# Performance work log

Measured on AMD Instinct MI355X. Metric: run time of the kernel, lower is better.

## Reference

```python
import jax, jax.numpy as jnp
import numpy as np

B = 32; SEQ = 900; GRID = 30; PFX = 16; D = 512
H = 8; HD = 64; WS = 3; SS = 1
NW = (GRID // WS) ** 2; N = WS * WS
INTER = 1536  # find_multiple(round(4.0*512*2/3), 256)
EPS = 1e-5
SCALE = HD ** -0.5


def _rel_pos_index():
    coords = np.stack(np.meshgrid(np.arange(WS), np.arange(WS), indexing='ij')).reshape(2, -1)
    rel = (coords[:, :, None] - coords[:, None, :]).transpose(1, 2, 0).copy()
    rel[:, :, 0] += WS - 1
    rel[:, :, 1] += WS - 1
    rel[:, :, 0] *= 2 * WS - 1
    return rel.sum(-1)  # [N, N]


def _attn_mask():
    img = np.zeros((GRID, GRID))
    cnt = 0
    sl = (slice(0, -WS), slice(-WS, -SS), slice(-SS, None))
    for h in sl:
        for w in sl:
            img[h, w] = cnt
            cnt += 1
    mw = img.reshape(GRID // WS, WS, GRID // WS, WS).transpose(0, 2, 1, 3).reshape(-1, N)
    diff = mw[:, None, :] - mw[:, :, None]
    return np.where(diff != 0, -100.0, 0.0).astype(np.float32)  # [nW, N, N]


REL_IDX = _rel_pos_index()
MASK = _attn_mask()


def rms_norm(x):
    xf = x.astype(jnp.float32)
    v = jnp.mean(xf * xf, -1, keepdims=True)
    return (xf * jax.lax.rsqrt(v + EPS)).astype(x.dtype)


def swiglu(x, gu_w, down_w):
    gu = x @ gu_w.T
    gate, up = gu[..., :INTER], gu[..., INTER:]
    return (jax.nn.silu(gate) * up) @ down_w.T


def setup_inputs() -> dict:
    key = jax.random.key(0)
    ks = jax.random.split(key, 8)
    s = 0.02
    return {
        'hidden_states': jax.random.normal(ks[0], (B, PFX + SEQ, D), jnp.float32),
        'qkv_w': jax.random.normal(ks[1], (3 * D, D), jnp.float32) * s,
        'qkv_b': jnp.zeros((3 * D,), jnp.float32),
        'proj_w': jax.random.normal(ks[2], (D, D), jnp.float32) * s,
        'proj_b': jnp.zeros((D,), jnp.float32),
        'rel_bias': jax.random.normal(ks[3], ((2 * WS - 1) ** 2, H), jnp.float32) * s,
        'gu_w': jax.random.normal(ks[4], (2 * INTER, D), jnp.float32) * s,
        'down_w': jax.random.normal(ks[5], (D, INTER), jnp.float32) * s,
        'pgu_w': jax.random.normal(ks[6], (2 * INTER, D), jnp.float32) * s,
        'pdown_w': jax.random.normal(ks[7], (D, INTER), jnp.float32) * s,
    }


def reference(hidden_states, qkv_w, qkv_b, proj_w, proj_b, rel_bias, gu_w, down_w, pgu_w, pdown_w):
    hs = hidden_states
    prefix = hs[:, :PFX]                                     # [B, 16, D]
    grid = hs[:, PFX:] + jnp.mean(prefix, 1, keepdims=True)  # broadcast prefix mean
    x = grid.reshape(B, GRID, GRID, D)
    residual = x
    # cyclic shift
    x = jnp.roll(x, (-SS, -SS), (1, 2))
    # window partition -> [B*nW, N, D]
    xw = x.reshape(B, GRID // WS, WS, GRID // WS, WS, D).transpose(0, 1, 3, 2, 4, 5).reshape(B * NW, N, D)
    qkv = (xw @ qkv_w.T + qkv_b).reshape(B * NW, N, 3, H, HD).transpose(2, 0, 3, 1, 4)
    q, k, v = qkv[0] * SCALE, qkv[1], qkv[2]                 # [B*nW, H, N, HD]
    attn = jnp.einsum('whid,whjd->whij', q, k)
    bias = rel_bias[jnp.asarray(REL_IDX).reshape(-1)].reshape(N, N, H).transpose(2, 0, 1)
    attn = attn + bias[None]
    attn = attn.reshape(B, NW, H, N, N) + jnp.asarray(MASK)[None, :, None]
    attn = jax.nn.softmax(attn.reshape(B * NW, H, N, N), -1)
    out = jnp.einsum('whij,whjd->whid', attn, v).transpose(0, 2, 1, 3).reshape(B * NW, N, D)
    out = out @ proj_w.T + proj_b
    # window reverse + reverse shift
    x = out.reshape(B, GRID // WS, GRID // WS, WS, WS, D).transpose(0, 1, 3, 2, 4, 5).reshape(B, GRID, GRID, D)
    x = jnp.roll(x, (SS, SS), (1, 2))
    x = rms_norm(residual.reshape(B, SEQ, D) + x.reshape(B, SEQ, D))
    prefix = rms_norm(prefix + swiglu(prefix, pgu_w, pdown_w))
    hs = jnp.concatenate([prefix, x], 1)
    return rms_norm(hs + swiglu(hs, gu_w, down_w))
```

## Files before the change

### kernel.cpp

```cpp
#include <hip/hip_runtime.h>
#include <cstdint>
#include <cstddef>

typedef float f32x4 __attribute__((ext_vector_type(4)));
typedef short s16x8 __attribute__((ext_vector_type(8)));
typedef short s16x4 __attribute__((ext_vector_type(4)));

#define DEV static __device__ __forceinline__

DEV float bf2f(short s) {
  union { unsigned u; float f; } c;
  c.u = ((unsigned)(unsigned short)s) << 16;
  return c.f;
}
DEV short f2bf(float f) {
  union { float f; unsigned u; } c;
  c.f = f;
  unsigned r = c.u + 0x7fffu + ((c.u >> 16) & 1u);
  return (short)(r >> 16);
}
DEV float wave_allsum(float v) {
#pragma unroll
  for (int off = 32; off > 0; off >>= 1) v += __shfl_xor(v, off, 64);
  return v;
}
DEV void gload_lds16(const void* g, void* l) {
  __builtin_amdgcn_global_load_lds(
      (const __attribute__((address_space(1))) void*)g,
      (__attribute__((address_space(3))) void*)l, 16, 0, 0);
}
DEV float silu_f(float g) { return g / (1.f + __expf(-g)); }

DEV int xcd_swizzle(int orig, int nwg) {
  int q = nwg >> 3, r = nwg & 7;
  int xcd = orig & 7, pos = orig >> 3;
  return (xcd < r ? xcd * (q + 1) : r * (q + 1) + (xcd - r) * q) + pos;
}

DEV void sync_phase() {
  asm volatile("s_waitcnt vmcnt(0)" ::: "memory");
  __builtin_amdgcn_s_barrier();
  __builtin_amdgcn_sched_barrier(0);
}

enum { EPI_BF16 = 0, EPI_BIAS_BF16 = 1, EPI_SCATTER = 4, EPI_GU = 6 };

template <int EPI>
__global__ __launch_bounds__(512, 2) void gemm8(
    const short* __restrict__ A, const short* __restrict__ W,
    const float* __restrict__ bias, void* __restrict__ outp,
    int M, int N, int K)
{
  __shared__ short lds[65536];
  const int tid = threadIdx.x;
  const int wid = tid >> 6, lane = tid & 63;
  const int wr = wid >> 2, wc = wid & 3;
  const int nwg = gridDim.x * gridDim.y;
  const int orig = blockIdx.y * gridDim.x + blockIdx.x;
  const int wg = xcd_swizzle(orig, nwg);
  const int bx = wg % gridDim.x, by = wg / gridDim.x;
  const int row0 = by * 256;
  const int c0 = bx * 256;

  f32x4 acc[8][4];
#pragma unroll
  for (int m = 0; m < 8; ++m)
#pragma unroll
    for (int n = 0; n < 4; ++n) acc[m][n] = f32x4{0.f, 0.f, 0.f, 0.f};

  const int srow = tid >> 3;
  const int k8s = (tid & 7) ^ (srow & 7);
  const short* aub[4];
  const short* bub[4];
#pragma unroll
  for (int u = 0; u < 4; ++u) {
    aub[u] = A + (size_t)(row0 + u * 64 + srow) * K + k8s * 8;
    bub[u] = W + (size_t)(c0 + u * 64 + srow) * K + k8s * 8;
  }
  const int ldw = wid * 512;

#define SA(d, u, kt) gload_lds16(aub[u] + (kt), &lds[(d)*16384 + (u)*4096 + ldw])
#define SB(d, u, kt) gload_lds16(bub[u] + (kt), &lds[32768 + (d)*16384 + (u)*4096 + ldw])
#define GATE(VN)                                              \
  asm volatile("s_waitcnt vmcnt(" #VN ")" ::: "memory");      \
  __builtin_amdgcn_s_barrier();                               \
  __builtin_amdgcn_sched_barrier(0);

  const int kg0 = (lane >> 4) ^ (lane & 7);
  const int kg1 = (4 + (lane >> 4)) ^ (lane & 7);
  const int aoff = (wr * 128 + (lane & 15)) * 64;
  const int boff = 32768 + (wc * 64 + (lane & 15)) * 64;

#define READ_B(d)                                                              \
  _Pragma("unroll") for (int n = 0; n < 4; ++n) {                              \
    bfr[0][n] = *(const s16x8*)&lds[(d)*16384 + boff + n * 1024 + kg0 * 8];    \
    bfr[1][n] = *(const s16x8*)&lds[(d)*16384 + boff + n * 1024 + kg1 * 8];    \
  }
#define DO_PHASE(d, p)                                                         \
  do {                                                                         \
    s16x8 a00 = *(const s16x8*)&lds[(d)*16384 + aoff + (2*(p))*1024 + kg0*8];  \
    s16x8 a01 = *(const s16x8*)&lds[(d)*16384 + aoff + (2*(p))*1024 + kg1*8];  \
    s16x8 a10 = *(const s16x8*)&lds[(d)*16384 + aoff + (2*(p)+1)*1024 + kg0*8];\
    s16x8 a11 = *(const s16x8*)&lds[(d)*16384 + aoff + (2*(p)+1)*1024 + kg1*8];\
    __builtin_amdgcn_s_setprio(1);                                             \
    _Pragma("unroll") for (int n = 0; n < 4; ++n)                              \
      acc[2*(p)][n] = __builtin_amdgcn_mfma_f32_16x16x32_bf16(a00, bfr[0][n], acc[2*(p)][n], 0, 0, 0); \
    _Pragma("unroll") for (int n = 0; n < 4; ++n)                              \
      acc[2*(p)+1][n] = __builtin_amdgcn_mfma_f32_16x16x32_bf16(a10, bfr[0][n], acc[2*(p)+1][n], 0, 0, 0); \
    _Pragma("unroll") for (int n = 0; n < 4; ++n)                              \
      acc[2*(p)][n] = __builtin_amdgcn_mfma_f32_16x16x32_bf16(a01, bfr[1][n], acc[2*(p)][n], 0, 0, 0); \
    _Pragma("unroll") for (int n = 0; n < 4; ++n)                              \
      acc[2*(p)+1][n] = __builtin_amdgcn_mfma_f32_16x16x32_bf16(a11, bfr[1][n], acc[2*(p)+1][n], 0, 0, 0); \
    __builtin_amdgcn_s_setprio(0);                                             \
  } while (0)

  SB(0, 0, 0); SB(0, 1, 0); SB(0, 2, 0); SB(0, 3, 0);
  SA(0, 0, 0); SA(0, 2, 0); SA(0, 1, 0); SA(0, 3, 0);

  const int NT = K >> 6;
  for (int t = 0; t < NT - 1; ++t) {
    const int d = t & 1, d1 = d ^ 1;
    const int kn = (t + 1) * 64;
    s16x8 bfr[2][4];
    SB(d1, 0, kn); SB(d1, 1, kn);
    GATE(4);
    READ_B(d);
    DO_PHASE(d, 0);
    SB(d1, 2, kn); SB(d1, 3, kn);
    DO_PHASE(d, 1);
    SA(d1, 0, kn); SA(d1, 2, kn);
    GATE(6);
    DO_PHASE(d, 2);
    SA(d1, 1, kn); SA(d1, 3, kn);
    DO_PHASE(d, 3);
  }
  {
    const int d = (NT - 1) & 1;
    s16x8 bfr[2][4];
    GATE(2);
    READ_B(d);
    DO_PHASE(d, 0);
    DO_PHASE(d, 1);
    GATE(0);
    DO_PHASE(d, 2);
    DO_PHASE(d, 3);
  }
#undef SA
#undef SB
#undef READ_B
#undef DO_PHASE

  const int li = lane >> 4, lc = lane & 15;
#pragma unroll
  for (int m = 0; m < 8; ++m) {
#pragma unroll
    for (int i = 0; i < 4; ++i) {
      int gr = row0 + wr * 128 + m * 16 + li * 4 + i;
      if (gr >= M) continue;
      size_t orow;
      if (EPI == EPI_SCATTER) {
        int b = gr / 900, rem = gr % 900;
        int w = rem / 9, n_ = rem % 9;
        int wi = w / 10, wj = w % 10;
        int ii = n_ / 3, jj = n_ % 3;
        int gy = wi * 3 + ii + 1; if (gy >= 30) gy -= 30;
        int gx = wj * 3 + jj + 1; if (gx >= 30) gx -= 30;
        orow = (size_t)b * 900 + gy * 30 + gx;
      } else {
        orow = (size_t)gr;
      }
#pragma unroll
      for (int n = 0; n < 4; ++n) {
        int gc = c0 + wc * 64 + n * 16 + lc;
        float v = acc[m][n][i];
        if (EPI == EPI_BIAS_BF16 || EPI == EPI_SCATTER) v += bias[gc];
        ((short*)outp)[orow * (size_t)N + gc] = f2bf(v);
      }
    }
  }
}

__global__ __launch_bounds__(512, 2) void gemm8gu(
    const short* __restrict__ A, const short* __restrict__ Wg,
    const short* __restrict__ Wu, short* __restrict__ outp, int M, int K)
{
  __shared__ short lds[65536];
  const int tid = threadIdx.x;
  const int wid = tid >> 6, lane = tid & 63;
  const int wr = wid >> 1, wc = wid & 1;
  const int nwg = gridDim.x * gridDim.y;
  const int orig = blockIdx.y * gridDim.x + blockIdx.x;
  const int wg = xcd_swizzle(orig, nwg);
  const int bx = wg % gridDim.x, by = wg / gridDim.x;
  const int row0 = by * 256;
  const int colg = bx * 128;

  f32x4 accg[4][4], accu[4][4];
#pragma unroll
  for (int m = 0; m < 4; ++m)
#pragma unroll
    for (int n = 0; n < 4; ++n) {
      accg[m][n] = f32x4{0.f, 0.f, 0.f, 0.f};
      accu[m][n] = f32x4{0.f, 0.f, 0.f, 0.f};
    }

  const int srow = tid >> 3;
  const int k8s = (tid & 7) ^ (srow & 7);
  const short* aub[4];
  const short* bub[4];
#pragma unroll
  for (int u = 0; u < 4; ++u)
    aub[u] = A + (size_t)(row0 + u * 64 + srow) * K + k8s * 8;
#pragma unroll
  for (int u = 0; u < 2; ++u) {
    bub[u]     = Wg + (size_t)(colg + u * 64 + srow) * K + k8s * 8;
    bub[u + 2] = Wu + (size_t)(colg + u * 64 + srow) * K + k8s * 8;
  }
  const int ldw = wid * 512;

#define SA(d, u, kt) gload_lds16(aub[u] + (kt), &lds[(d)*16384 + (u)*4096 + ldw])
#define SB(d, u, kt) gload_lds16(bub[u] + (kt), &lds[32768 + (d)*16384 + (u)*4096 + ldw])
#define GATE(VN)                                              \
  asm volatile("s_waitcnt vmcnt(" #VN ")" ::: "memory");      \
  __builtin_amdgcn_s_barrier();                               \
  __builtin_amdgcn_sched_barrier(0);

  const int kg0 = (lane >> 4) ^ (lane & 7);
  const int kg1 = (4 + (lane >> 4)) ^ (lane & 7);
  const int aoff = (wr * 64 + (lane & 15)) * 64;
  const int bgoff = 32768 + (wc * 64 + (lane & 15)) * 64;
  const int buoff = 32768 + (128 + wc * 64 + (lane & 15)) * 64;

#define READ_BF(d, BOFF, BF)                                                   \
  _Pragma("unroll") for (int n = 0; n < 4; ++n) {                              \
    BF[0][n] = *(const s16x8*)&lds[(d)*16384 + (BOFF) + n * 1024 + kg0 * 8];   \
    BF[1][n] = *(const s16x8*)&lds[(d)*16384 + (BOFF) + n * 1024 + kg1 * 8];   \
  }
#define READ_A(d)                                                              \
  _Pragma("unroll") for (int m = 0; m < 4; ++m) {                              \
    af[0][m] = *(const s16x8*)&lds[(d)*16384 + aoff + m * 1024 + kg0 * 8];     \
    af[1][m] = *(const s16x8*)&lds[(d)*16384 + aoff + m * 1024 + kg1 * 8];     \
  }
#define MM2(BF, h, ACC)                                                        \
  do {                                                                         \
    __builtin_amdgcn_s_setprio(1);                                             \
    _Pragma("unroll") for (int n = 0; n < 4; ++n)                              \
      ACC[2*(h)][n] = __builtin_amdgcn_mfma_f32_16x16x32_bf16(af[0][2*(h)], BF[0][n], ACC[2*(h)][n], 0, 0, 0); \
    _Pragma("unroll") for (int n = 0; n < 4; ++n)                              \
      ACC[2*(h)+1][n] = __builtin_amdgcn_mfma_f32_16x16x32_bf16(af[0][2*(h)+1], BF[0][n], ACC[2*(h)+1][n], 0, 0, 0); \
    _Pragma("unroll") for (int n = 0; n < 4; ++n)                              \
      ACC[2*(h)][n] = __builtin_amdgcn_mfma_f32_16x16x32_bf16(af[1][2*(h)], BF[1][n], ACC[2*(h)][n], 0, 0, 0); \
    _Pragma("unroll") for (int n = 0; n < 4; ++n)                              \
      ACC[2*(h)+1][n] = __builtin_amdgcn_mfma_f32_16x16x32_bf16(af[1][2*(h)+1], BF[1][n], ACC[2*(h)+1][n], 0, 0, 0); \
    __builtin_amdgcn_s_setprio(0);                                             \
  } while (0)

  SA(0, 0, 0); SA(0, 1, 0); SA(0, 2, 0); SA(0, 3, 0);
  SB(0, 0, 0); SB(0, 1, 0); SB(0, 2, 0); SB(0, 3, 0);

  const int NT = K >> 6;
  for (int t = 0; t < NT - 1; ++t) {
    const int d = t & 1, d1 = d ^ 1;
    const int kn = (t + 1) * 64;
    s16x8 af[2][4], bg[2][4], bu[2][4];
    GATE(2);
    READ_BF(d, bgoff, bg);
    READ_A(d);
    MM2(bg, 0, accg);
    SA(d1, 0, kn); SA(d1, 1, kn);
    MM2(bg, 1, accg);
    SA(d1, 2, kn); SA(d1, 3, kn);
    GATE(4);
    READ_BF(d, buoff, bu);
    MM2(bu, 0, accu);
    SB(d1, 0, kn); SB(d1, 1, kn);
    MM2(bu, 1, accu);
    SB(d1, 2, kn); SB(d1, 3, kn);
  }
  {
    const int d = (NT - 1) & 1;
    s16x8 af[2][4], bg[2][4], bu[2][4];
    GATE(2);
    READ_BF(d, bgoff, bg);
    READ_A(d);
    MM2(bg, 0, accg);
    MM2(bg, 1, accg);
    GATE(0);
    READ_BF(d, buoff, bu);
    MM2(bu, 0, accu);
    MM2(bu, 1, accu);
  }
#undef SA
#undef SB
#undef READ_BF
#undef READ_A
#undef MM2
#undef GATE

  const int li = lane >> 4, lc = lane & 15;
#pragma unroll
  for (int m = 0; m < 4; ++m) {
#pragma unroll
    for (int i = 0; i < 4; ++i) {
      int gr = row0 + wr * 64 + m * 16 + li * 4 + i;
      if (gr >= M) continue;
#pragma unroll
      for (int n = 0; n < 4; ++n) {
        int gc = colg + wc * 64 + n * 16 + lc;
        outp[(size_t)gr * 1536 + gc] = f2bf(silu_f(accg[m][n][i]) * accu[m][n][i]);
      }
    }
  }
}

template <int EPI>
__global__ __launch_bounds__(256) void gemm2(
    const short* __restrict__ A, const short* __restrict__ W,
    const short* __restrict__ Wu, const float* __restrict__ bias,
    void* __restrict__ outp, int M, int N, int K)
{
  __shared__ short As0[8192], Bs0[8192];
  __shared__ short As1[8192], Bs1[8192];
  const int tid = threadIdx.x;
  const int wave = tid >> 6, lane = tid & 63;
  const int nwg = gridDim.x * gridDim.y;
  const int orig = blockIdx.y * gridDim.x + blockIdx.x;
  const int wg = xcd_swizzle(orig, nwg);
  const int bx = wg % gridDim.x, by = wg / gridDim.x;
  const int row0 = by * 128;
  const int col0 = (EPI == EPI_GU) ? bx * 64 : bx * 128;
  const int wr = wave >> 1, wc = wave & 1;

  f32x4 acc[4][4];
#pragma unroll
  for (int m = 0; m < 4; ++m)
#pragma unroll
    for (int n = 0; n < 4; ++n) acc[m][n] = f32x4{0.f, 0.f, 0.f, 0.f};

  const short* aptr[4];
  const short* bptr[4];
  int ldst[4];
#pragma unroll
  for (int i = 0; i < 4; ++i) {
    int e = i * 2048 + tid * 8;
    int srow = e >> 6;
    int skg = ((e >> 3) & 7) ^ (srow & 7);
    aptr[i] = A + (size_t)(row0 + srow) * K + skg * 8;
    if (EPI == EPI_GU)
      bptr[i] = (srow < 64 ? W + (size_t)(col0 + srow) * K
                           : Wu + (size_t)(col0 + srow - 64) * K) + skg * 8;
    else
      bptr[i] = W + (size_t)(col0 + srow) * K + skg * 8;
    ldst[i] = i * 2048 + wave * 512;
  }

#define STAGE(AS, BS, KT)                                   \
  do {                                                      \
    _Pragma("unroll") for (int i = 0; i < 4; ++i)           \
        gload_lds16(aptr[i] + (KT), &AS[ldst[i]]);          \
    _Pragma("unroll") for (int i = 0; i < 4; ++i)           \
        gload_lds16(bptr[i] + (KT), &BS[ldst[i]]);          \
  } while (0)

#define COMPUTE(AS, BS)                                                        \
  do {                                                                         \
    _Pragma("unroll") for (int ks = 0; ks < 2; ++ks) {                         \
      s16x8 af[4], bfr[4];                                                     \
      _Pragma("unroll") for (int m = 0; m < 4; ++m) {                          \
        int row = wr * 64 + m * 16 + (lane & 15);                              \
        int kg = (ks * 4 + (lane >> 4)) ^ (row & 7);                           \
        af[m] = *(const s16x8*)&AS[row * 64 + kg * 8];                         \
      }                                                                        \
      _Pragma("unroll") for (int n = 0; n < 4; ++n) {                          \
        int brow = (EPI == EPI_GU)                                             \
                       ? ((n < 2 ? wc * 32 + n * 16                            \
                                 : 64 + wc * 32 + (n - 2) * 16) + (lane & 15)) \
                       : (wc * 64 + n * 16 + (lane & 15));                     \
        int kg = (ks * 4 + (lane >> 4)) ^ (brow & 7);                          \
        bfr[n] = *(const s16x8*)&BS[brow * 64 + kg * 8];                       \
      }                                                                        \
      _Pragma("unroll") for (int m = 0; m < 4; ++m)                            \
          _Pragma("unroll") for (int n = 0; n < 4; ++n)                        \
              acc[m][n] = __builtin_amdgcn_mfma_f32_16x16x32_bf16(             \
                  af[m], bfr[n], acc[m][n], 0, 0, 0);                          \
    }                                                                          \
  } while (0)

  STAGE(As0, Bs0, 0);
  sync_phase();
  for (int kt = 0; kt < K; kt += 128) {
    STAGE(As1, Bs1, kt + 64);
    COMPUTE(As0, Bs0);
    sync_phase();
    if (kt + 128 < K) STAGE(As0, Bs0, kt + 128);
    COMPUTE(As1, Bs1);
    if (kt + 128 < K) sync_phase();
  }
#undef STAGE
#undef COMPUTE

  const int lr = (lane >> 4) * 4, lc = lane & 15;
#pragma unroll
  for (int m = 0; m < 4; ++m) {
#pragma unroll
    for (int i = 0; i < 4; ++i) {
      int gr = row0 + wr * 64 + m * 16 + lr + i;
      if (EPI == EPI_GU) {
#pragma unroll
        for (int n = 0; n < 2; ++n) {
          int gc = col0 + wc * 32 + n * 16 + lc;
          float v = silu_f(acc[m][n][i]) * acc[m][n + 2][i];
          ((short*)outp)[(size_t)gr * N + gc] = f2bf(v);
        }
      } else {
#pragma unroll
        for (int n = 0; n < 4; ++n) {
          int gc = col0 + wc * 64 + n * 16 + lc;
          ((short*)outp)[(size_t)gr * N + gc] = f2bf(acc[m][n][i]);
        }
      }
    }
  }
}

__global__ __launch_bounds__(256) void cvt_all_kernel(
    const float* __restrict__ s_qkv, const float* __restrict__ s_proj,
    const float* __restrict__ s_gu, const float* __restrict__ s_down,
    const float* __restrict__ s_pgu, const float* __restrict__ s_pdown,
    short* __restrict__ dst) {
  int i = blockIdx.x * 256 + threadIdx.x;
  if (i >= 1441792) return;
  const float* src;
  int base;
  if (i < 262144) {
    if (i < 196608) { src = s_qkv; base = 0; }
    else            { src = s_proj; base = 196608; }
  } else if (i < 851968) {
    if (i < 655360) { src = s_gu; base = 262144; }
    else            { src = s_down; base = 655360; }
  } else {
    if (i < 1245184) { src = s_pgu; base = 851968; }
    else             { src = s_pdown; base = 1245184; }
  }
  f32x4 v = *(const f32x4*)(src + (size_t)(i - base) * 4);
  s16x4 o;
#pragma unroll
  for (int e = 0; e < 4; ++e) o[e] = f2bf(v[e]);
  *(s16x4*)(dst + (size_t)i * 4) = o;
}

__global__ __launch_bounds__(256) void prefix_cvt_kernel(const float* __restrict__ hs,
                                                         short* __restrict__ dst) {
  int i = blockIdx.x * 256 + threadIdx.x;
  if (i >= 512 * 128) return;
  int r = i >> 7, c4 = i & 127;
  int b = r >> 4, t = r & 15;
  f32x4 v = *(const f32x4*)(hs + ((size_t)b * 916 + t) * 512 + c4 * 4);
  s16x4 o;
#pragma unroll
  for (int e = 0; e < 4; ++e) o[e] = f2bf(v[e]);
  *(s16x4*)(dst + (size_t)r * 512 + c4 * 4) = o;
}

__global__ __launch_bounds__(512) void mean_kernel(const float* __restrict__ hs,
                                                   float* __restrict__ m) {
  int b = blockIdx.x, d = threadIdx.x;
  float s = 0.f;
#pragma unroll
  for (int t = 0; t < 16; ++t) s += hs[((size_t)b * 916 + t) * 512 + d];
  m[b * 512 + d] = s * (1.f / 16.f);
}

__global__ __launch_bounds__(256) void prep_kernel(const float* __restrict__ hs,
                                                   const float* __restrict__ m,
                                                   short* __restrict__ xw) {
  int idx = blockIdx.x * 256 + threadIdx.x;
  if (idx >= 32 * 900 * 128) return;
  int c4 = idx & 127;
  int row = idx >> 7;
  int b = row / 900, rem = row % 900;
  int gy = rem / 30, gx = rem % 30;
  f32x4 v = *(const f32x4*)(hs + ((size_t)b * 916 + 16 + rem) * 512 + c4 * 4);
  f32x4 mm = *(const f32x4*)(m + b * 512 + c4 * 4);
  v += mm;
  int ry = gy + 29; if (ry >= 30) ry -= 30;
  int rx = gx + 29; if (rx >= 30) rx -= 30;
  int wi = ry / 3, ii = ry % 3, wj = rx / 3, jj = rx % 3;
  size_t xrow = (size_t)((b * 100 + wi * 10 + wj) * 9 + ii * 3 + jj);
  s16x4 o;
#pragma unroll
  for (int e = 0; e < 4; ++e) o[e] = f2bf(v[e]);
  *(s16x4*)(xw + xrow * 512 + c4 * 4) = o;
}

__global__ __launch_bounds__(256) void attn_kernel(const short* __restrict__ qkv,
                                                   const float* __restrict__ rel_bias,
                                                   short* __restrict__ outp) {
  __shared__ short sq[9 * 512];
  __shared__ short sk[9 * 512];
  __shared__ short sv[9 * 512];
  __shared__ float sS[648];
  const int wlin = blockIdx.x;
  const int w = wlin % 100;
  const int wi = w / 10, wj = w % 10;
  const int tid = threadIdx.x;
  const short* base = qkv + (size_t)wlin * 9 * 1536;
  for (int idx = tid; idx < 1728; idx += 256) {
    int n = idx / 192, c8 = idx % 192;
    s16x8 v = *(const s16x8*)(base + (size_t)n * 1536 + c8 * 8);
    int which = c8 >> 6;
    short* dst = (which == 0) ? sq : (which == 1) ? sk : sv;
    *(s16x8*)(dst + n * 512 + (c8 & 63) * 8) = v;
  }
  __syncthreads();
  for (int idx = tid; idx < 648; idx += 256) {
    int h = idx / 81, r = idx % 81, i = r / 9, j = r % 9;
    const short* qp = sq + i * 512 + h * 64;
    const short* kp = sk + j * 512 + h * 64;
    float dot = 0.f;
#pragma unroll
    for (int c = 0; c < 8; ++c) {
      s16x8 qv = *(const s16x8*)(qp + c * 8);
      s16x8 kv = *(const s16x8*)(kp + c * 8);
#pragma unroll
      for (int e = 0; e < 8; ++e) dot += bf2f(qv[e]) * bf2f(kv[e]);
    }
    float s = dot * 0.125f;
    int ia = i / 3, ja = i % 3, ib = j / 3, jb = j % 3;
    s += rel_bias[(5 * (ia - ib + 2) + (ja - jb + 2)) * 8 + h];
    int ra = wi * 3 + ia, ca = wj * 3 + ja, rb = wi * 3 + ib, cb = wj * 3 + jb;
    int rga = (ra < 27) ? 0 : (ra < 29) ? 1 : 2;
    int cga = (ca < 27) ? 0 : (ca < 29) ? 1 : 2;
    int rgb = (rb < 27) ? 0 : (rb < 29) ? 1 : 2;
    int cgb = (cb < 27) ? 0 : (cb < 29) ? 1 : 2;
    if (rga * 3 + cga != rgb * 3 + cgb) s -= 100.f;
    sS[idx] = s;
  }
  __syncthreads();
  if (tid < 72) {
    float* row = sS + tid * 9;
    float mx = row[0];
#pragma unroll
    for (int j = 1; j < 9; ++j) mx = fmaxf(mx, row[j]);
    float e[9], sum = 0.f;
#pragma unroll
    for (int j = 0; j < 9; ++j) { e[j] = __expf(row[j] - mx); sum += e[j]; }
    float inv = 1.f / sum;
#pragma unroll
    for (int j = 0; j < 9; ++j) row[j] = e[j] * inv;
  }
  __syncthreads();
  for (int idx = tid; idx < 576; idx += 256) {
    int h = idx / 72, r = idx % 72, i = r / 8, d8 = r % 8;
    const float* p = sS + (h * 9 + i) * 9;
    float a[8] = {0, 0, 0, 0, 0, 0, 0, 0};
#pragma unroll
    for (int j = 0; j < 9; ++j) {
      float pj = p[j];
      s16x8 vv = *(const s16x8*)(sv + j * 512 + h * 64 + d8 * 8);
#pragma unroll
      for (int e = 0; e < 8; ++e) a[e] += pj * bf2f(vv[e]);
    }
    s16x8 o;
#pragma unroll
    for (int e = 0; e < 8; ++e) o[e] = f2bf(a[e]);
    *(s16x8*)(outp + ((size_t)wlin * 9 + i) * 512 + h * 64 + d8 * 8) = o;
  }
}

__global__ __launch_bounds__(256) void addnorm1_kernel(const short* __restrict__ xw,
                                                       const short* __restrict__ p,
                                                       float* __restrict__ out,
                                                       short* __restrict__ hsb) {
  int row = blockIdx.x * 4 + (threadIdx.x >> 6);
  int lane = threadIdx.x & 63;
  int b_ = row / 900, rem = row % 900;
  int gy = rem / 30, gx = rem % 30;
  int ry = gy + 29; if (ry >= 30) ry -= 30;
  int rx = gx + 29; if (rx >= 30) rx -= 30;
  size_t xrow = (size_t)((b_ * 100 + (ry / 3) * 10 + rx / 3) * 9 + (ry % 3) * 3 + rx % 3);
  s16x8 a8 = *(const s16x8*)(xw + xrow * 512 + lane * 8);
  s16x8 b8 = *(const s16x8*)(p + (size_t)row * 512 + lane * 8);
  float x[8];
  float ss = 0.f;
#pragma unroll
  for (int e = 0; e < 8; ++e) {
    x[e] = bf2f(a8[e]) + bf2f(b8[e]);
    ss += x[e] * x[e];
  }
  ss = wave_allsum(ss);
  float sc = rsqrtf(ss * (1.f / 512.f) + 1e-5f);
  size_t orow = ((size_t)b_ * 916 + 16 + rem) * 512 + lane * 8;
  s16x8 o;
#pragma unroll
  for (int e = 0; e < 8; ++e) {
    x[e] *= sc;
    o[e] = f2bf(x[e]);
  }
  *(f32x4*)(out + orow) = f32x4{x[0], x[1], x[2], x[3]};
  *(f32x4*)(out + orow + 4) = f32x4{x[4], x[5], x[6], x[7]};
  *(s16x8*)(hsb + orow) = o;
}

__global__ __launch_bounds__(256) void prefix_addnorm_kernel(const float* __restrict__ hs,
                                                             const short* __restrict__ pd,
                                                             float* __restrict__ out,
                                                             short* __restrict__ hsb) {
  int r = blockIdx.x * 4 + (threadIdx.x >> 6);
  int lane = threadIdx.x & 63;
  int b = r >> 4, t = r & 15;
  size_t orow = ((size_t)b * 916 + t) * 512 + lane * 8;
  f32x4 a0 = *(const f32x4*)(hs + orow);
  f32x4 a1 = *(const f32x4*)(hs + orow + 4);
  s16x8 d8 = *(const s16x8*)(pd + (size_t)r * 512 + lane * 8);
  float x[8];
  float ss = 0.f;
#pragma unroll
  for (int e = 0; e < 8; ++e) {
    x[e] = (e < 4 ? a0[e] : a1[e - 4]) + bf2f(d8[e]);
    ss += x[e] * x[e];
  }
  ss = wave_allsum(ss);
  float sc = rsqrtf(ss * (1.f / 512.f) + 1e-5f);
  s16x8 o;
#pragma unroll
  for (int e = 0; e < 8; ++e) {
    x[e] *= sc;
    o[e] = f2bf(x[e]);
  }
  *(f32x4*)(out + orow) = f32x4{x[0], x[1], x[2], x[3]};
  *(f32x4*)(out + orow + 4) = f32x4{x[4], x[5], x[6], x[7]};
  *(s16x8*)(hsb + orow) = o;
}

__global__ __launch_bounds__(256) void final_addnorm_kernel(const short* __restrict__ dn,
                                                            float* __restrict__ io) {
  int row = blockIdx.x * 4 + (threadIdx.x >> 6);
  int lane = threadIdx.x & 63;
  size_t off = (size_t)row * 512 + lane * 8;
  f32x4 a0 = *(const f32x4*)(io + off);
  f32x4 a1 = *(const f32x4*)(io + off + 4);
  s16x8 d8 = *(const s16x8*)(dn + off);
  float x[8];
  float ss = 0.f;
#pragma unroll
  for (int e = 0; e < 8; ++e) {
    x[e] = (e < 4 ? a0[e] : a1[e - 4]) + bf2f(d8[e]);
    ss += x[e] * x[e];
  }
  ss = wave_allsum(ss);
  float sc = rsqrtf(ss * (1.f / 512.f) + 1e-5f);
#pragma unroll
  for (int e = 0; e < 8; ++e) x[e] *= sc;
  *(f32x4*)(io + off) = f32x4{x[0], x[1], x[2], x[3]};
  *(f32x4*)(io + off + 4) = f32x4{x[4], x[5], x[6], x[7]};
}

static constexpr size_t OFF_WQKV   = 0;
static constexpr size_t OFF_WPROJ  = 1572864;
static constexpr size_t OFF_WGU    = 2097152;
static constexpr size_t OFF_WDOWN  = 5242880;
static constexpr size_t OFF_WPGU   = 6815744;
static constexpr size_t OFF_WPDOWN = 9961472;
static constexpr size_t OFF_MEAN   = 11534336;
static constexpr size_t OFF_PREFB  = 11599872;
static constexpr size_t OFF_PINTER = 13697024;
static constexpr size_t OFF_PDOUT  = 15269888;
static constexpr size_t OFF_XW     = 16777216;
static constexpr size_t OFF_QKV    = 46399488;
static constexpr size_t OFF_ATTNO  = 134873088;
static constexpr size_t OFF_PROJS  = OFF_QKV;
static constexpr size_t OFF_INTER  = OFF_XW;
static constexpr size_t OFF_HSB    = 164364288;
static constexpr size_t OFF_DNOUT  = OFF_ATTNO;

extern "C" void kernel_launch(void* const* d_in, const int* in_sizes, int n_in,
                              void* d_out, int out_size, void* d_ws, size_t ws_size,
                              hipStream_t stream) {
  const float* hs      = (const float*)d_in[0];
  const float* qkv_w   = (const float*)d_in[1];
  const float* qkv_b   = (const float*)d_in[2];
  const float* proj_w  = (const float*)d_in[3];
  const float* proj_b  = (const float*)d_in[4];
  const float* rel_b   = (const float*)d_in[5];
  const float* gu_w    = (const float*)d_in[6];
  const float* down_w  = (const float*)d_in[7];
  const float* pgu_w   = (const float*)d_in[8];
  const float* pdown_w = (const float*)d_in[9];

  char* ws = (char*)d_ws;
  short* Wqkv   = (short*)(ws + OFF_WQKV);
  short* Wproj  = (short*)(ws + OFF_WPROJ);
  short* Wgu    = (short*)(ws + OFF_WGU);
  short* Wdown  = (short*)(ws + OFF_WDOWN);
  short* Wpgu   = (short*)(ws + OFF_WPGU);
  short* Wpdown = (short*)(ws + OFF_WPDOWN);
  float* meanb  = (float*)(ws + OFF_MEAN);
  short* prefb  = (short*)(ws + OFF_PREFB);
  short* pinter = (short*)(ws + OFF_PINTER);
  short* pdout  = (short*)(ws + OFF_PDOUT);
  short* xw     = (short*)(ws + OFF_XW);
  short* qkvb   = (short*)(ws + OFF_QKV);
  short* attno  = (short*)(ws + OFF_ATTNO);
  short* projs  = (short*)(ws + OFF_PROJS);
  short* interb = (short*)(ws + OFF_INTER);
  short* hsb    = (short*)(ws + OFF_HSB);
  short* dnout  = (short*)(ws + OFF_DNOUT);
  float* outf   = (float*)d_out;

  cvt_all_kernel<<<5632, 256, 0, stream>>>(qkv_w, proj_w, gu_w, down_w,
                                           pgu_w, pdown_w, (short*)ws);
  prefix_cvt_kernel<<<256, 256, 0, stream>>>(hs, prefb);

  mean_kernel<<<32, 512, 0, stream>>>(hs, meanb);
  prep_kernel<<<14400, 256, 0, stream>>>(hs, meanb, xw);

  gemm8<EPI_BIAS_BF16><<<dim3(6, 113), 512, 0, stream>>>(
      xw, Wqkv, qkv_b, qkvb, 28800, 1536, 512);
  attn_kernel<<<3200, 256, 0, stream>>>(qkvb, rel_b, attno);

  gemm8<EPI_SCATTER><<<dim3(2, 113), 512, 0, stream>>>(
      attno, Wproj, proj_b, projs, 28800, 512, 512);
  addnorm1_kernel<<<7200, 256, 0, stream>>>(xw, projs, outf, hsb);

  gemm2<EPI_GU><<<dim3(24, 4), 256, 0, stream>>>(
      prefb, Wpgu, Wpgu + 1536 * 512, nullptr, pinter, 512, 1536, 512);
  gemm2<EPI_BF16><<<dim3(4, 4), 256, 0, stream>>>(
      pinter, Wpdown, nullptr, nullptr, pdout, 512, 512, 1536);
  prefix_addnorm_kernel<<<128, 256, 0, stream>>>(hs, pdout, outf, hsb);

  gemm8gu<<<dim3(12, 115), 512, 0, stream>>>(
      hsb, Wgu, Wgu + 1536 * 512, interb, 29312, 512);
  gemm8<EPI_BF16><<<dim3(2, 115), 512, 0, stream>>>(
      interb, Wdown, nullptr, dnout, 29312, 512, 1536);
  final_addnorm_kernel<<<7328, 256, 0, stream>>>(dnout, outf);

  (void)in_sizes; (void)n_in; (void)out_size; (void)ws_size;
}
```

Before: 425.7 us.

## Fuse residual add and RMSNorm into full-row proj and down GEMM epilogues

Adds a gemm_norm kernel whose blocks each own 64 full 512-wide output rows. This lets the epilogue add the bias and residual, compute the RMSNorm through a cross-wave LDS reduction, and write the final float and bf16 outputs directly. It replaces the proj GEMM plus addnorm1 and the down GEMM plus final_addnorm, removing two bf16 intermediate round-trips and two launches. The cost is smaller 64-row tiles with 1-block occupancy, lower grid parallelism (450/458 blocks) and a larger weight slab staged per k-step, which may cut GEMM efficiency.

```diff
diff --git a/kernel.cpp b/kernel.cpp
--- a/kernel.cpp
+++ b/kernel.cpp
@@ -43,7 +43,7 @@
   __builtin_amdgcn_sched_barrier(0);
 }
 
-enum { EPI_BF16 = 0, EPI_BIAS_BF16 = 1, EPI_SCATTER = 4, EPI_GU = 6 };
+enum { EPI_BF16 = 0, EPI_BIAS_BF16 = 1, EPI_GU = 6 };
 
 template <int EPI>
 __global__ __launch_bounds__(512, 2) void gemm8(
@@ -157,24 +157,12 @@
     for (int i = 0; i < 4; ++i) {
       int gr = row0 + wr * 128 + m * 16 + li * 4 + i;
       if (gr >= M) continue;
-      size_t orow;
-      if (EPI == EPI_SCATTER) {
-        int b = gr / 900, rem = gr % 900;
-        int w = rem / 9, n_ = rem % 9;
-        int wi = w / 10, wj = w % 10;
-        int ii = n_ / 3, jj = n_ % 3;
-        int gy = wi * 3 + ii + 1; if (gy >= 30) gy -= 30;
-        int gx = wj * 3 + jj + 1; if (gx >= 30) gx -= 30;
-        orow = (size_t)b * 900 + gy * 30 + gx;
-      } else {
-        orow = (size_t)gr;
-      }
 #pragma unroll
       for (int n = 0; n < 4; ++n) {
         int gc = c0 + wc * 64 + n * 16 + lc;
         float v = acc[m][n][i];
-        if (EPI == EPI_BIAS_BF16 || EPI == EPI_SCATTER) v += bias[gc];
-        ((short*)outp)[orow * (size_t)N + gc] = f2bf(v);
+        if (EPI == EPI_BIAS_BF16) v += bias[gc];
+        ((short*)outp)[(size_t)gr * N + gc] = f2bf(v);
       }
     }
   }
@@ -220,10 +208,6 @@
 
 #define SA(d, u, kt) gload_lds16(aub[u] + (kt), &lds[(d)*16384 + (u)*4096 + ldw])
 #define SB(d, u, kt) gload_lds16(bub[u] + (kt), &lds[32768 + (d)*16384 + (u)*4096 + ldw])
-#define GATE(VN)                                              \
-  asm volatile("s_waitcnt vmcnt(" #VN ")" ::: "memory");      \
-  __builtin_amdgcn_s_barrier();                               \
-  __builtin_amdgcn_sched_barrier(0);
 
   const int kg0 = (lane >> 4) ^ (lane & 7);
   const int kg1 = (4 + (lane >> 4)) ^ (lane & 7);
@@ -254,6 +238,10 @@
       ACC[2*(h)+1][n] = __builtin_amdgcn_mfma_f32_16x16x32_bf16(af[1][2*(h)+1], BF[1][n], ACC[2*(h)+1][n], 0, 0, 0); \
     __builtin_amdgcn_s_setprio(0);                                             \
   } while (0)
+#define GATE(VN)                                              \
+  asm volatile("s_waitcnt vmcnt(" #VN ")" ::: "memory");      \
+  __builtin_amdgcn_s_barrier();                               \
+  __builtin_amdgcn_sched_barrier(0);
 
   SA(0, 0, 0); SA(0, 1, 0); SA(0, 2, 0); SA(0, 3, 0);
   SB(0, 0, 0); SB(0, 1, 0); SB(0, 2, 0); SB(0, 3, 0);
@@ -308,6 +296,144 @@
       for (int n = 0; n < 4; ++n) {
         int gc = colg + wc * 64 + n * 16 + lc;
         outp[(size_t)gr * 1536 + gc] = f2bf(silu_f(accg[m][n][i]) * accu[m][n][i]);
+      }
+    }
+  }
+}
+
+template <int PROJ>
+__global__ __launch_bounds__(512, 1) void gemm_norm(
+    const short* __restrict__ A, const short* __restrict__ W,
+    const float* __restrict__ bias, const short* __restrict__ residb,
+    float* __restrict__ outf, short* __restrict__ hsb, int K)
+{
+  __shared__ short lds[73728];
+  const int tid = threadIdx.x;
+  const int wid = tid >> 6, lane = tid & 63;
+  const int wr = wid >> 2, wc = wid & 3;
+  const int row0 = blockIdx.x * 64;
+  const int tid8 = tid * 8;
+
+  f32x4 acc[2][8];
+#pragma unroll
+  for (int m = 0; m < 2; ++m)
+#pragma unroll
+    for (int n = 0; n < 8; ++n) acc[m][n] = f32x4{0.f, 0.f, 0.f, 0.f};
+
+  const int srow = tid >> 3;
+  const int k8s = (tid & 7) ^ (srow & 7);
+  const short* aptr = A + (size_t)(row0 + srow) * K + k8s * 8;
+  const short* bptr[8];
+#pragma unroll
+  for (int u = 0; u < 8; ++u)
+    bptr[u] = W + (size_t)(u * 64 + srow) * K + k8s * 8;
+
+#define STG(d, kt)                                                          \
+  do {                                                                      \
+    gload_lds16(aptr + (kt), &lds[(d)*4096 + tid8]);                        \
+    _Pragma("unroll") for (int u = 0; u < 8; ++u)                           \
+        gload_lds16(bptr[u] + (kt), &lds[8192 + (d)*32768 + u*4096 + tid8]);\
+  } while (0)
+#define GATEN(VN)                                             \
+  asm volatile("s_waitcnt vmcnt(" #VN ")" ::: "memory");      \
+  __builtin_amdgcn_s_barrier();                               \
+  __builtin_amdgcn_sched_barrier(0);
+
+  const int kg0 = (lane >> 4) ^ (lane & 7);
+  const int kg1 = (4 + (lane >> 4)) ^ (lane & 7);
+  const int arow = (wr * 32 + (lane & 15)) * 64;
+  const int brow = (wc * 128 + (lane & 15)) * 64;
+
+  STG(0, 0);
+  const int NT = K >> 6;
+  for (int t = 0; t < NT; ++t) {
+    const int d = t & 1;
+    if (t + 1 < NT) {
+      STG(d ^ 1, (t + 1) * 64);
+      GATEN(9);
+    } else {
+      GATEN(0);
+    }
+    s16x8 af0[2], af1[2], bf0[8], bf1[8];
+#pragma unroll
+    for (int m = 0; m < 2; ++m) {
+      af0[m] = *(const s16x8*)&lds[d * 4096 + arow + m * 1024 + kg0 * 8];
+      af1[m] = *(const s16x8*)&lds[d * 4096 + arow + m * 1024 + kg1 * 8];
+    }
+#pragma unroll
+    for (int n = 0; n < 8; ++n) {
+      bf0[n] = *(const s16x8*)&lds[8192 + d * 32768 + brow + n * 1024 + kg0 * 8];
+      bf1[n] = *(const s16x8*)&lds[8192 + d * 32768 + brow + n * 1024 + kg1 * 8];
+    }
+    __builtin_amdgcn_s_setprio(1);
+#pragma unroll
+    for (int m = 0; m < 2; ++m)
+#pragma unroll
+      for (int n = 0; n < 8; ++n)
+        acc[m][n] = __builtin_amdgcn_mfma_f32_16x16x32_bf16(af0[m], bf0[n], acc[m][n], 0, 0, 0);
+#pragma unroll
+    for (int m = 0; m < 2; ++m)
+#pragma unroll
+      for (int n = 0; n < 8; ++n)
+        acc[m][n] = __builtin_amdgcn_mfma_f32_16x16x32_bf16(af1[m], bf1[n], acc[m][n], 0, 0, 0);
+    __builtin_amdgcn_s_setprio(0);
+    __builtin_amdgcn_s_barrier();
+  }
+#undef STG
+#undef GATEN
+
+  const int li = lane >> 4, lc = lane & 15;
+  float* fbuf = (float*)lds;
+#pragma unroll
+  for (int m = 0; m < 2; ++m) {
+#pragma unroll
+    for (int i = 0; i < 4; ++i) {
+      int rowl = wr * 32 + m * 16 + li * 4 + i;
+      int gr = row0 + rowl;
+      float s = 0.f;
+#pragma unroll
+      for (int n = 0; n < 8; ++n) {
+        int gc = wc * 128 + n * 16 + lc;
+        float v = acc[m][n][i];
+        if (PROJ) v += bias[gc] + bf2f(residb[(size_t)gr * 512 + gc]);
+        else      v += outf[(size_t)gr * 512 + gc];
+        acc[m][n][i] = v;
+        s += v * v;
+      }
+      s += __shfl_xor(s, 1, 64);
+      s += __shfl_xor(s, 2, 64);
+      s += __shfl_xor(s, 4, 64);
+      s += __shfl_xor(s, 8, 64);
+      if (lc == 0) fbuf[rowl * 4 + wc] = s;
+    }
+  }
+  __builtin_amdgcn_s_barrier();
+#pragma unroll
+  for (int m = 0; m < 2; ++m) {
+#pragma unroll
+    for (int i = 0; i < 4; ++i) {
+      int rowl = wr * 32 + m * 16 + li * 4 + i;
+      int gr = row0 + rowl;
+      float tot = fbuf[rowl * 4] + fbuf[rowl * 4 + 1] + fbuf[rowl * 4 + 2] + fbuf[rowl * 4 + 3];
+      float sc = rsqrtf(tot * (1.f / 512.f) + 1e-5f);
+      size_t orow;
+      if (PROJ) {
+        int b = gr / 900, rem = gr % 900;
+        int w = rem / 9, n_ = rem % 9;
+        int wi = w / 10, wj = w % 10;
+        int ii = n_ / 3, jj = n_ % 3;
+        int gy = wi * 3 + ii + 1; if (gy >= 30) gy -= 30;
+        int gx = wj * 3 + jj + 1; if (gx >= 30) gx -= 30;
+        orow = ((size_t)b * 916 + 16 + gy * 30 + gx);
+      } else {
+        orow = (size_t)gr;
+      }
+#pragma unroll
+      for (int n = 0; n < 8; ++n) {
+        int gc = wc * 128 + n * 16 + lc;
+        float v = acc[m][n][i] * sc;
+        outf[orow * 512 + gc] = v;
+        if (PROJ) hsb[orow * 512 + gc] = f2bf(v);
       }
     }
   }
@@ -568,40 +694,6 @@
   }
 }
 
-__global__ __launch_bounds__(256) void addnorm1_kernel(const short* __restrict__ xw,
-                                                       const short* __restrict__ p,
-                                                       float* __restrict__ out,
-                                                       short* __restrict__ hsb) {
-  int row = blockIdx.x * 4 + (threadIdx.x >> 6);
-  int lane = threadIdx.x & 63;
-  int b_ = row / 900, rem = row % 900;
-  int gy = rem / 30, gx = rem % 30;
-  int ry = gy + 29; if (ry >= 30) ry -= 30;
-  int rx = gx + 29; if (rx >= 30) rx -= 30;
-  size_t xrow = (size_t)((b_ * 100 + (ry / 3) * 10 + rx / 3) * 9 + (ry % 3) * 3 + rx % 3);
-  s16x8 a8 = *(const s16x8*)(xw + xrow * 512 + lane * 8);
-  s16x8 b8 = *(const s16x8*)(p + (size_t)row * 512 + lane * 8);
-  float x[8];
-  float ss = 0.f;
-#pragma unroll
-  for (int e = 0; e < 8; ++e) {
-    x[e] = bf2f(a8[e]) + bf2f(b8[e]);
-    ss += x[e] * x[e];
-  }
-  ss = wave_allsum(ss);
-  float sc = rsqrtf(ss * (1.f / 512.f) + 1e-5f);
-  size_t orow = ((size_t)b_ * 916 + 16 + rem) * 512 + lane * 8;
-  s16x8 o;
-#pragma unroll
-  for (int e = 0; e < 8; ++e) {
-    x[e] *= sc;
-    o[e] = f2bf(x[e]);
-  }
-  *(f32x4*)(out + orow) = f32x4{x[0], x[1], x[2], x[3]};
-  *(f32x4*)(out + orow + 4) = f32x4{x[4], x[5], x[6], x[7]};
-  *(s16x8*)(hsb + orow) = o;
-}
-
 __global__ __launch_bounds__(256) void prefix_addnorm_kernel(const float* __restrict__ hs,
                                                              const short* __restrict__ pd,
                                                              float* __restrict__ out,
@@ -633,29 +725,6 @@
   *(s16x8*)(hsb + orow) = o;
 }
 
-__global__ __launch_bounds__(256) void final_addnorm_kernel(const short* __restrict__ dn,
-                                                            float* __restrict__ io) {
-  int row = blockIdx.x * 4 + (threadIdx.x >> 6);
-  int lane = threadIdx.x & 63;
-  size_t off = (size_t)row * 512 + lane * 8;
-  f32x4 a0 = *(const f32x4*)(io + off);
-  f32x4 a1 = *(const f32x4*)(io + off + 4);
-  s16x8 d8 = *(const s16x8*)(dn + off);
-  float x[8];
-  float ss = 0.f;
-#pragma unroll
-  for (int e = 0; e < 8; ++e) {
-    x[e] = (e < 4 ? a0[e] : a1[e - 4]) + bf2f(d8[e]);
-    ss += x[e] * x[e];
-  }
-  ss = wave_allsum(ss);
-  float sc = rsqrtf(ss * (1.f / 512.f) + 1e-5f);
-#pragma unroll
-  for (int e = 0; e < 8; ++e) x[e] *= sc;
-  *(f32x4*)(io + off) = f32x4{x[0], x[1], x[2], x[3]};
-  *(f32x4*)(io + off + 4) = f32x4{x[4], x[5], x[6], x[7]};
-}
-
 static constexpr size_t OFF_WQKV   = 0;
 static constexpr size_t OFF_WPROJ  = 1572864;
 static constexpr size_t OFF_WGU    = 2097152;
@@ -669,10 +738,8 @@
 static constexpr size_t OFF_XW     = 16777216;
 static constexpr size_t OFF_QKV    = 46399488;
 static constexpr size_t OFF_ATTNO  = 134873088;
-static constexpr size_t OFF_PROJS  = OFF_QKV;
 static constexpr size_t OFF_INTER  = OFF_XW;
 static constexpr size_t OFF_HSB    = 164364288;
-static constexpr size_t OFF_DNOUT  = OFF_ATTNO;
 
 extern "C" void kernel_launch(void* const* d_in, const int* in_sizes, int n_in,
                               void* d_out, int out_size, void* d_ws, size_t ws_size,
@@ -702,10 +769,8 @@
   short* xw     = (short*)(ws + OFF_XW);
   short* qkvb   = (short*)(ws + OFF_QKV);
   short* attno  = (short*)(ws + OFF_ATTNO);
-  short* projs  = (short*)(ws + OFF_PROJS);
   short* interb = (short*)(ws + OFF_INTER);
   short* hsb    = (short*)(ws + OFF_HSB);
-  short* dnout  = (short*)(ws + OFF_DNOUT);
   float* outf   = (float*)d_out;
 
   cvt_all_kernel<<<5632, 256, 0, stream>>>(qkv_w, proj_w, gu_w, down_w,
@@ -719,9 +784,7 @@
       xw, Wqkv, qkv_b, qkvb, 28800, 1536, 512);
   attn_kernel<<<3200, 256, 0, stream>>>(qkvb, rel_b, attno);
 
-  gemm8<EPI_SCATTER><<<dim3(2, 113), 512, 0, stream>>>(
-      attno, Wproj, proj_b, projs, 28800, 512, 512);
-  addnorm1_kernel<<<7200, 256, 0, stream>>>(xw, projs, outf, hsb);
+  gemm_norm<1><<<450, 512, 0, stream>>>(attno, Wproj, proj_b, xw, outf, hsb, 512);
 
   gemm2<EPI_GU><<<dim3(24, 4), 256, 0, stream>>>(
       prefb, Wpgu, Wpgu + 1536 * 512, nullptr, pinter, 512, 1536, 512);
@@ -731,9 +794,8 @@
 
   gemm8gu<<<dim3(12, 115), 512, 0, stream>>>(
       hsb, Wgu, Wgu + 1536 * 512, interb, 29312, 512);
-  gemm8<EPI_BF16><<<dim3(2, 115), 512, 0, stream>>>(
-      interb, Wdown, nullptr, dnout, 29312, 512, 1536);
-  final_addnorm_kernel<<<7328, 256, 0, stream>>>(dnout, outf);
+  gemm_norm<0><<<458, 512, 0, stream>>>(interb, Wdown, nullptr, nullptr, outf,
+                                        nullptr, 1536);
 
   (void)in_sizes; (void)n_in; (void)out_size; (void)ws_size;
 }
```

Result: slower. 450.3 us (+5.8%).

## Shrink gate/up SwiGLU GEMM tile to 64 rows with 256-thread blocks

Applied to the files above, without the earlier changes.

Reworks the fused gate/up GEMM so each workgroup covers 64 rows × 128 gate + 128 up columns with 4 waves instead of 256 rows with 8 waves. LDS use drops and the grid grows fourfold, aiming for better occupancy and load balance across CUs. The cost is lower arithmetic intensity: each workgroup streams the same B weight tile for only 64 rows, so weight traffic per flop rises. The wait-count gating and load schedule are rewritten to match the new load counts.

```diff
diff --git a/kernel.cpp b/kernel.cpp
--- a/kernel.cpp
+++ b/kernel.cpp
@@ -149,6 +149,7 @@
 #undef SB
 #undef READ_B
 #undef DO_PHASE
+#undef GATE
 
   const int li = lane >> 4, lc = lane & 15;
 #pragma unroll
@@ -180,46 +181,61 @@
   }
 }
 
-__global__ __launch_bounds__(512, 2) void gemm8gu(
+__global__ __launch_bounds__(256, 2) void gemm8gu(
     const short* __restrict__ A, const short* __restrict__ Wg,
     const short* __restrict__ Wu, short* __restrict__ outp, int M, int K)
 {
-  __shared__ short lds[65536];
+  __shared__ short lds[40960];
   const int tid = threadIdx.x;
-  const int wid = tid >> 6, lane = tid & 63;
-  const int wr = wid >> 1, wc = wid & 1;
+  const int w = tid >> 6, lane = tid & 63;
+  const int wr = w >> 1, wc = w & 1;
   const int nwg = gridDim.x * gridDim.y;
   const int orig = blockIdx.y * gridDim.x + blockIdx.x;
   const int wg = xcd_swizzle(orig, nwg);
   const int bx = wg % gridDim.x, by = wg / gridDim.x;
-  const int row0 = by * 256;
+  const int row0 = by * 64;
   const int colg = bx * 128;
 
-  f32x4 accg[4][4], accu[4][4];
-#pragma unroll
-  for (int m = 0; m < 4; ++m)
+  f32x4 accg[2][4], accu[2][4];
+#pragma unroll
+  for (int m = 0; m < 2; ++m)
 #pragma unroll
     for (int n = 0; n < 4; ++n) {
       accg[m][n] = f32x4{0.f, 0.f, 0.f, 0.f};
       accu[m][n] = f32x4{0.f, 0.f, 0.f, 0.f};
     }
 
-  const int srow = tid >> 3;
-  const int k8s = (tid & 7) ^ (srow & 7);
-  const short* aub[4];
-  const short* bub[4];
-#pragma unroll
-  for (int u = 0; u < 4; ++u)
-    aub[u] = A + (size_t)(row0 + u * 64 + srow) * K + k8s * 8;
-#pragma unroll
-  for (int u = 0; u < 2; ++u) {
-    bub[u]     = Wg + (size_t)(colg + u * 64 + srow) * K + k8s * 8;
-    bub[u + 2] = Wu + (size_t)(colg + u * 64 + srow) * K + k8s * 8;
-  }
-  const int ldw = wid * 512;
-
-#define SA(d, u, kt) gload_lds16(aub[u] + (kt), &lds[(d)*16384 + (u)*4096 + ldw])
-#define SB(d, u, kt) gload_lds16(bub[u] + (kt), &lds[32768 + (d)*16384 + (u)*4096 + ldw])
+  const short* aptr[2];
+#pragma unroll
+  for (int i = 0; i < 2; ++i) {
+    int r = (i * 4 + w) * 8 + (lane >> 3);
+    int k8 = (lane & 7) ^ (r & 7);
+    aptr[i] = A + (size_t)(row0 + r) * K + k8 * 8;
+  }
+  const short* bptr[8];
+#pragma unroll
+  for (int j = 0; j < 8; ++j) {
+    int br = (j * 4 + w) * 8 + (lane >> 3);
+    int k8 = (lane & 7) ^ (br & 7);
+    bptr[j] = (br < 128 ? Wg + (size_t)(colg + br) * K
+                        : Wu + (size_t)(colg + br - 128) * K) + k8 * 8;
+  }
+
+#define SAV(d, kt)                                                         \
+  do {                                                                     \
+    gload_lds16(aptr[0] + (kt), &lds[(d)*4096 + w * 512]);                 \
+    gload_lds16(aptr[1] + (kt), &lds[(d)*4096 + 2048 + w * 512]);          \
+  } while (0)
+#define SBG(d, kt)                                                         \
+  do {                                                                     \
+    _Pragma("unroll") for (int j = 0; j < 4; ++j)                          \
+        gload_lds16(bptr[j] + (kt), &lds[8192 + (d)*16384 + (j*4 + w)*512]);\
+  } while (0)
+#define SBU(d, kt)                                                         \
+  do {                                                                     \
+    _Pragma("unroll") for (int j = 4; j < 8; ++j)                          \
+        gload_lds16(bptr[j] + (kt), &lds[8192 + (d)*16384 + (j*4 + w)*512]);\
+  } while (0)
 #define GATE(VN)                                              \
   asm volatile("s_waitcnt vmcnt(" #VN ")" ::: "memory");      \
   __builtin_amdgcn_s_barrier();                               \
@@ -227,82 +243,77 @@
 
   const int kg0 = (lane >> 4) ^ (lane & 7);
   const int kg1 = (4 + (lane >> 4)) ^ (lane & 7);
-  const int aoff = (wr * 64 + (lane & 15)) * 64;
-  const int bgoff = 32768 + (wc * 64 + (lane & 15)) * 64;
-  const int buoff = 32768 + (128 + wc * 64 + (lane & 15)) * 64;
-
+  const int aoff = (wr * 32 + (lane & 15)) * 64;
+  const int bgoff = 8192 + (wc * 64 + (lane & 15)) * 64;
+  const int buoff = bgoff + 8192;
+
+#define READ_A(d)                                                              \
+  _Pragma("unroll") for (int m = 0; m < 2; ++m) {                              \
+    af[0][m] = *(const s16x8*)&lds[(d)*4096 + aoff + m * 1024 + kg0 * 8];      \
+    af[1][m] = *(const s16x8*)&lds[(d)*4096 + aoff + m * 1024 + kg1 * 8];      \
+  }
 #define READ_BF(d, BOFF, BF)                                                   \
   _Pragma("unroll") for (int n = 0; n < 4; ++n) {                              \
     BF[0][n] = *(const s16x8*)&lds[(d)*16384 + (BOFF) + n * 1024 + kg0 * 8];   \
     BF[1][n] = *(const s16x8*)&lds[(d)*16384 + (BOFF) + n * 1024 + kg1 * 8];   \
   }
-#define READ_A(d)                                                              \
-  _Pragma("unroll") for (int m = 0; m < 4; ++m) {                              \
-    af[0][m] = *(const s16x8*)&lds[(d)*16384 + aoff + m * 1024 + kg0 * 8];     \
-    af[1][m] = *(const s16x8*)&lds[(d)*16384 + aoff + m * 1024 + kg1 * 8];     \
-  }
-#define MM2(BF, h, ACC)                                                        \
+#define MMH(BF, g, ACC)                                                        \
   do {                                                                         \
     __builtin_amdgcn_s_setprio(1);                                             \
-    _Pragma("unroll") for (int n = 0; n < 4; ++n)                              \
-      ACC[2*(h)][n] = __builtin_amdgcn_mfma_f32_16x16x32_bf16(af[0][2*(h)], BF[0][n], ACC[2*(h)][n], 0, 0, 0); \
-    _Pragma("unroll") for (int n = 0; n < 4; ++n)                              \
-      ACC[2*(h)+1][n] = __builtin_amdgcn_mfma_f32_16x16x32_bf16(af[0][2*(h)+1], BF[0][n], ACC[2*(h)+1][n], 0, 0, 0); \
-    _Pragma("unroll") for (int n = 0; n < 4; ++n)                              \
-      ACC[2*(h)][n] = __builtin_amdgcn_mfma_f32_16x16x32_bf16(af[1][2*(h)], BF[1][n], ACC[2*(h)][n], 0, 0, 0); \
-    _Pragma("unroll") for (int n = 0; n < 4; ++n)                              \
-      ACC[2*(h)+1][n] = __builtin_amdgcn_mfma_f32_16x16x32_bf16(af[1][2*(h)+1], BF[1][n], ACC[2*(h)+1][n], 0, 0, 0); \
+    _Pragma("unroll") for (int m = 0; m < 2; ++m)                              \
+        _Pragma("unroll") for (int n = 0; n < 4; ++n)                          \
+            ACC[m][n] = __builtin_amdgcn_mfma_f32_16x16x32_bf16(               \
+                af[g][m], BF[g][n], ACC[m][n], 0, 0, 0);                       \
     __builtin_amdgcn_s_setprio(0);                                             \
   } while (0)
 
-  SA(0, 0, 0); SA(0, 1, 0); SA(0, 2, 0); SA(0, 3, 0);
-  SB(0, 0, 0); SB(0, 1, 0); SB(0, 2, 0); SB(0, 3, 0);
+  SAV(0, 0); SBG(0, 0); SBU(0, 0);
 
   const int NT = K >> 6;
   for (int t = 0; t < NT - 1; ++t) {
     const int d = t & 1, d1 = d ^ 1;
     const int kn = (t + 1) * 64;
-    s16x8 af[2][4], bg[2][4], bu[2][4];
-    GATE(2);
+    s16x8 af[2][2], bg[2][4], bu[2][4];
+    GATE(4);
+    READ_A(d);
     READ_BF(d, bgoff, bg);
-    READ_A(d);
-    MM2(bg, 0, accg);
-    SA(d1, 0, kn); SA(d1, 1, kn);
-    MM2(bg, 1, accg);
-    SA(d1, 2, kn); SA(d1, 3, kn);
-    GATE(4);
+    MMH(bg, 0, accg);
+    SAV(d1, kn);
+    MMH(bg, 1, accg);
+    SBG(d1, kn);
+    GATE(6);
     READ_BF(d, buoff, bu);
-    MM2(bu, 0, accu);
-    SB(d1, 0, kn); SB(d1, 1, kn);
-    MM2(bu, 1, accu);
-    SB(d1, 2, kn); SB(d1, 3, kn);
+    MMH(bu, 0, accu);
+    SBU(d1, kn);
+    MMH(bu, 1, accu);
   }
   {
     const int d = (NT - 1) & 1;
-    s16x8 af[2][4], bg[2][4], bu[2][4];
-    GATE(2);
+    s16x8 af[2][2], bg[2][4], bu[2][4];
+    GATE(4);
+    READ_A(d);
     READ_BF(d, bgoff, bg);
-    READ_A(d);
-    MM2(bg, 0, accg);
-    MM2(bg, 1, accg);
+    MMH(bg, 0, accg);
+    MMH(bg, 1, accg);
     GATE(0);
     READ_BF(d, buoff, bu);
-    MM2(bu, 0, accu);
-    MM2(bu, 1, accu);
-  }
-#undef SA
-#undef SB
+    MMH(bu, 0, accu);
+    MMH(bu, 1, accu);
+  }
+#undef SAV
+#undef SBG
+#undef SBU
+#undef READ_A
 #undef READ_BF
-#undef READ_A
-#undef MM2
+#undef MMH
 #undef GATE
 
   const int li = lane >> 4, lc = lane & 15;
 #pragma unroll
-  for (int m = 0; m < 4; ++m) {
+  for (int m = 0; m < 2; ++m) {
 #pragma unroll
     for (int i = 0; i < 4; ++i) {
-      int gr = row0 + wr * 64 + m * 16 + li * 4 + i;
+      int gr = row0 + wr * 32 + m * 16 + li * 4 + i;
       if (gr >= M) continue;
 #pragma unroll
       for (int n = 0; n < 4; ++n) {
@@ -729,7 +740,7 @@
       pinter, Wpdown, nullptr, nullptr, pdout, 512, 512, 1536);
   prefix_addnorm_kernel<<<128, 256, 0, stream>>>(hs, pdout, outf, hsb);
 
-  gemm8gu<<<dim3(12, 115), 512, 0, stream>>>(
+  gemm8gu<<<dim3(12, 458), 256, 0, stream>>>(
       hsb, Wgu, Wgu + 1536 * 512, interb, 29312, 512);
   gemm8<EPI_BF16><<<dim3(2, 115), 512, 0, stream>>>(
       interb, Wdown, nullptr, dnout, 29312, 512, 1536);
```

Result: slower. 439.2 us (+3.2%).
